# Optimization experiments

Measured on AMD Instinct MI355X. Metric: run time of the kernel, lower is better.

## Reference

```python
import jax, jax.numpy as jnp
import numpy as np

D_MODEL = 1024
D_K = 1024
B, T = 4, 2048


def setup_inputs() -> dict:
    key = jax.random.key(0)
    kx, kq, kk, kv = jax.random.split(key, 4)
    s = 1.0 / np.sqrt(D_MODEL)
    return {
        "x": jax.random.normal(kx, (B, T, D_MODEL), dtype=jnp.float32),
        "W_q": jax.random.normal(kq, (D_MODEL, D_K), dtype=jnp.float32) * s,
        "W_k": jax.random.normal(kk, (D_MODEL, D_K), dtype=jnp.float32) * s,
        "W_v": jax.random.normal(kv, (D_MODEL, D_K), dtype=jnp.float32) * s,
    }


def reference(x, W_q, W_k, W_v):
    # x: (B, T, C); W_*: (C, d_k). Linear(no bias) == x @ W
    q = jnp.einsum('btc,ck->btk', x, W_q)
    k = jnp.einsum('btc,ck->btk', x, W_k)
    v = jnp.einsum('btc,ck->btk', x, W_v)
    d_k = W_q.shape[1]
    scores = jnp.einsum('bqk,bsk->bqs', q, k) / jnp.sqrt(jnp.asarray(d_k, x.dtype))
    T_ = x.shape[1]
    causal = jnp.tril(jnp.ones((T_, T_), dtype=bool))
    scores = jnp.where(causal, scores, jnp.asarray(-jnp.inf, scores.dtype))
    weights = jax.nn.softmax(scores, axis=-1)
    return jnp.einsum('bqs,bsk->bqk', weights, v)
```

## Files before the change

kernel.cpp:

```cpp
#include <hip/hip_runtime.h>
#include <hip/hip_bf16.h>
#include <stdint.h>
#include <math.h>

typedef __bf16 bf16x8 __attribute__((ext_vector_type(8)));
typedef float  f32x4  __attribute__((ext_vector_type(4)));
typedef unsigned int u32x4 __attribute__((ext_vector_type(4)));

__device__ __forceinline__ unsigned short f2bf(float x) {
    union { float f; unsigned u; } v; v.f = x;
    unsigned r = v.u + 0x7fffu + ((v.u >> 16) & 1u);
    return (unsigned short)(r >> 16);
}

__device__ __forceinline__ float bf2f(unsigned short b) {
    union { unsigned u; float f; } v; v.u = ((unsigned)b) << 16; return v.f;
}

__device__ __forceinline__ void async16(const void* g, void* l) {
    __builtin_amdgcn_global_load_lds(
        (const __attribute__((address_space(1))) void*)g,
        (__attribute__((address_space(3))) void*)l,
        16, 0, 0);
}

template <typename OutT, bool KLIMIT, bool VFOLD, int ZMODE>
__global__ __launch_bounds__(256, 4) void gemm_bt(
    const unsigned short* __restrict__ A,
    const unsigned short* __restrict__ Bt,
    OutT* __restrict__ C,
    unsigned short* __restrict__ VtOut,
    int M, int N, int K, int lda, int ldb, int ldc,
    int ldvt, int nsplit,
    long long sA, long long sB, long long sC, long long sVt, float scale)
{
    int bn, bm, bz;
    if constexpr (ZMODE == 1) {
        const int o = blockIdx.x, x = o & 7, q = o >> 3;
        bz = x >> 1;
        const int tile = (x & 1) * 192 + q * 4 + blockIdx.z;
        bn = tile / 16; bm = tile % 16;
    } else if constexpr (ZMODE == 2) {
        const int o = blockIdx.x, x = o & 7, q = o >> 3;
        bz = x >> 1;
        const int t = (x & 1) * 68 + q * 4 + blockIdx.z;
        int r = (int)((sqrtf(8.f * (float)t + 1.f) - 1.f) * 0.5f);
        while ((r + 1) * (r + 2) / 2 <= t) r++;
        while (r * (r + 1) / 2 > t) r--;
        bm = r; bn = t - r * (r + 1) / 2;
    } else if constexpr (ZMODE == 3) {
        const int o = blockIdx.x, x = o & 7, q = o >> 3;
        bz = x >> 1;
        const int tile = (x & 1) * 64 + q * 4 + blockIdx.z;
        bn = tile >> 4; bm = 15 - (tile & 15);
    } else {
        bn = blockIdx.x;
        bm = KLIMIT ? (gridDim.y - 1 - blockIdx.y) : blockIdx.y;
        bz = blockIdx.z;
    }

    A  += (long long)bz * sA;
    Bt += (long long)bz * sB;
    C  += (long long)bz * sC;

    const int m0 = bm * 128, n0 = bn * 128;
    const int Keff = KLIMIT ? min(K, (bm + 1) * 128) : K;

    __shared__ __align__(16) unsigned short LDS[2 * 2 * 128 * 32];

    const int tid  = threadIdx.x;
    const int w    = tid >> 6, l = tid & 63;
    const int wr   = w >> 1,  wc = w & 1;
    const int lrow = l & 15,  quad = l >> 4;

    f32x4 acc[4][4] = {};

    const int rA0  = 32 * w + (l >> 2);
    const int cOff = (((l & 3) ^ ((l >> 3) & 3))) * 8;
    const unsigned short* aG0 = A  + (long long)(m0 + rA0)      * lda + cOff;
    const unsigned short* aG1 = A  + (long long)(m0 + rA0 + 16) * lda + cOff;
    const unsigned short* bG0 = Bt + (long long)(n0 + rA0)      * ldb + cOff;
    const unsigned short* bG1 = Bt + (long long)(n0 + rA0 + 16) * ldb + cOff;
    unsigned short* aL = &LDS[(2 * w) * 512 + l * 8];
    unsigned short* bL = aL + 4096;

    const int sl = (lrow >> 1) & 3;

    async16(aG0, aL);
    async16(aG1, aL + 512);
    async16(bG0, bL);
    async16(bG1, bL + 512);

    for (int k0 = 0; k0 < Keff; k0 += 32) {
        const int cur = ((k0 >> 5) & 1) * 8192;
        __syncthreads();

        if (k0 + 32 < Keff) {
            const int nxt = cur ^ 8192;
            async16(aG0 + k0 + 32, aL + nxt);
            async16(aG1 + k0 + 32, aL + nxt + 512);
            async16(bG0 + k0 + 32, bL + nxt);
            async16(bG1 + k0 + 32, bL + nxt + 512);
        }

        const unsigned short* As = &LDS[cur];
        const unsigned short* Bs = &LDS[cur + 4096];
        bf16x8 af[4], bfr[4];
#pragma unroll
        for (int i = 0; i < 4; i++) {
            af[i]  = *(const bf16x8*)&As[(wr * 64 + i * 16 + lrow) * 32 + (quad ^ sl) * 8];
            bfr[i] = *(const bf16x8*)&Bs[(wc * 64 + i * 16 + lrow) * 32 + (quad ^ sl) * 8];
        }
#pragma unroll
        for (int i = 0; i < 4; i++)
#pragma unroll
            for (int j = 0; j < 4; j++)
                acc[i][j] = __builtin_amdgcn_mfma_f32_16x16x32_bf16(af[i], bfr[j], acc[i][j], 0, 0, 0);
    }

    if constexpr (VFOLD) {
        if (n0 >= nsplit) {
            unsigned short* Vp = VtOut + (long long)bz * sVt;
#pragma unroll
            for (int i = 0; i < 4; i++) {
                const int t = m0 + wr * 64 + i * 16 + quad * 4;
#pragma unroll
                for (int j = 0; j < 4; j++) {
                    const int d = (n0 - nsplit) + wc * 64 + j * 16 + lrow;
                    union { unsigned short u[4]; uint2 p; } o;
#pragma unroll
                    for (int r = 0; r < 4; r++) o.u[r] = f2bf(acc[i][j][r] * scale);
                    *(uint2*)(Vp + (long long)d * ldvt + t) = o.p;
                }
            }
            return;
        }
    }

    __syncthreads();

    char* eb = (char*)LDS + w * 2288;
    const int erow = l >> 2, ep = l & 3;

    if constexpr (sizeof(OutT) == 2) {
#pragma unroll
        for (int i = 0; i < 4; i++) {
#pragma unroll
            for (int j = 0; j < 4; j++)
#pragma unroll
                for (int r = 0; r < 4; r++)
                    *(unsigned short*)(eb + (quad * 4 + r) * 144 + (j * 16 + lrow) * 2) =
                        f2bf(acc[i][j][r] * scale);
            const long long gm = m0 + wr * 64 + i * 16 + erow;
#pragma unroll
            for (int c = 0; c < 2; c++) {
                u32x4 d = *(u32x4*)(eb + erow * 144 + ep * 32 + c * 16);
                *(u32x4*)((unsigned short*)C + gm * ldc + (n0 + wc * 64 + ep * 16 + c * 8)) = d;
            }
        }
    } else {
#pragma unroll
        for (int i = 0; i < 4; i++) {
            const long long gm = m0 + wr * 64 + i * 16 + erow;
#pragma unroll
            for (int jc = 0; jc < 2; jc++) {
#pragma unroll
                for (int jj = 0; jj < 2; jj++)
#pragma unroll
                    for (int r = 0; r < 4; r++)
                        *(float*)(eb + (quad * 4 + r) * 144 + (jj * 16 + lrow) * 4) =
                            acc[i][2 * jc + jj][r] * scale;
#pragma unroll
                for (int c = 0; c < 2; c++) {
                    f32x4 d = *(f32x4*)(eb + erow * 144 + ep * 32 + c * 16);
                    *(f32x4*)((float*)C + gm * ldc + (n0 + wc * 64 + jc * 32 + ep * 8 + c * 4)) = d;
                }
            }
        }
    }
}

__global__ __launch_bounds__(256) void cast_f32_bf16(
    const float4* __restrict__ in, unsigned short* __restrict__ out, int n4)
{
    int i = blockIdx.x * 256 + threadIdx.x;
    if (i >= n4) return;
    float4 v = in[i];
    union { unsigned short u[4]; uint2 p; } o;
    o.u[0] = f2bf(v.x); o.u[1] = f2bf(v.y); o.u[2] = f2bf(v.z); o.u[3] = f2bf(v.w);
    *(uint2*)(out + (long long)i * 4) = o.p;
}

__global__ __launch_bounds__(256) void transpose_cast_w3(
    const float* __restrict__ W0, const float* __restrict__ W1,
    const float* __restrict__ W2, unsigned short* __restrict__ out, int n)
{
    const float* in = (blockIdx.z == 0) ? W0 : (blockIdx.z == 1) ? W1 : W2;
    out += (long long)blockIdx.z * n * n;
    __shared__ float tile[32][33];
    const int tx = threadIdx.x, ty = threadIdx.y;
    const int c0 = blockIdx.x * 32, r0 = blockIdx.y * 32;
#pragma unroll
    for (int i = 0; i < 4; i++)
        tile[ty + i * 8][tx] = in[(long long)(r0 + ty + i * 8) * n + c0 + tx];
    __syncthreads();
#pragma unroll
    for (int i = 0; i < 4; i++)
        out[(long long)(c0 + ty + i * 8) * n + r0 + tx] = f2bf(tile[tx][ty + i * 8]);
}

__global__ __launch_bounds__(256) void causal_softmax_bf16(
    const unsigned short* __restrict__ S, unsigned short* __restrict__ P, int T)
{
    const int row = blockIdx.x;
    const int t   = row & (T - 1);
    const int L   = t + 1;
    const unsigned short* s = S + (long long)row * T;
    unsigned short* p = P + (long long)row * T;
    const int tid  = threadIdx.x;
    const int base = tid * 8;

    uint4 raw = *(const uint4*)(s + base);
    unsigned rr[4] = {raw.x, raw.y, raw.z, raw.w};
    float v[8];
#pragma unroll
    for (int k = 0; k < 4; k++) {
        union { unsigned u; float f; } a, b;
        a.u = (rr[k] & 0xFFFFu) << 16;
        b.u = rr[k] & 0xFFFF0000u;
        v[2 * k] = a.f; v[2 * k + 1] = b.f;
    }
    float mx = -3.0e38f;
#pragma unroll
    for (int k = 0; k < 8; k++) {
        if (base + k >= L) v[k] = -3.0e38f;
        mx = fmaxf(mx, v[k]);
    }
#pragma unroll
    for (int off = 32; off; off >>= 1) mx = fmaxf(mx, __shfl_xor(mx, off));
    __shared__ float red[4], red2[4];
    const int wid = tid >> 6, lid = tid & 63;
    if (lid == 0) red[wid] = mx;
    __syncthreads();
    mx = fmaxf(fmaxf(red[0], red[1]), fmaxf(red[2], red[3]));

    float sum = 0.f;
#pragma unroll
    for (int k = 0; k < 8; k++) { v[k] = __expf(v[k] - mx); sum += v[k]; }
#pragma unroll
    for (int off = 32; off; off >>= 1) sum += __shfl_xor(sum, off);
    if (lid == 0) red2[wid] = sum;
    __syncthreads();
    sum = red2[0] + red2[1] + red2[2] + red2[3];
    const float inv = 1.0f / sum;

    union { unsigned short u[8]; uint4 q; } o;
#pragma unroll
    for (int k = 0; k < 8; k++) o.u[k] = f2bf(v[k] * inv);
    *(uint4*)(p + base) = o.q;
}

extern "C" void kernel_launch(void* const* d_in, const int* in_sizes, int n_in,
                              void* d_out, int out_size, void* d_ws, size_t ws_size,
                              hipStream_t stream)
{
    const int B = 4, T = 2048, C = 1024, D = 1024;
    const float* x  = (const float*)d_in[0];
    const float* Wq = (const float*)d_in[1];
    const float* Wk = (const float*)d_in[2];
    const float* Wv = (const float*)d_in[3];
    float* out = (float*)d_out;
    char* ws = (char*)d_ws;

    const size_t MB = 1ull << 20;
    unsigned short* Xbf   = (unsigned short*)(ws + 0);
    unsigned short* WqkvT = (unsigned short*)(ws + 16 * MB);
    unsigned short* QK    = (unsigned short*)(ws + 22 * MB);
    unsigned short* Vt    = (unsigned short*)(ws + 54 * MB);
    unsigned short* Sbf   = (unsigned short*)(ws + 70 * MB);
    unsigned short* P     = (unsigned short*)(ws + 0);

    const long long sX  = (long long)T * C;
    const long long sQK = (long long)T * 2 * D;
    const long long sVt = (long long)D * T;
    const long long sS  = (long long)T * T;
    const long long sO  = (long long)T * D;

    {
        int n4 = B * T * C / 4;
        cast_f32_bf16<<<dim3((n4 + 255) / 256), dim3(256), 0, stream>>>(
            (const float4*)x, Xbf, n4);
    }
    {
        dim3 g(32, 32, 3), b(32, 8);
        transpose_cast_w3<<<g, b, 0, stream>>>(Wq, Wk, Wv, WqkvT, 1024);
    }
    {
        dim3 g(384, 1, 4), b(256);
        gemm_bt<unsigned short, false, true, 1><<<g, b, 0, stream>>>(
            Xbf, WqkvT, QK, Vt, 2048, 3072, 1024, 1024, 1024, 2048,
             T,  2048, sX, 0, sQK, sVt, 1.0f);
    }
    {
        dim3 g(136, 1, 4), b(256);
        gemm_bt<unsigned short, false, false, 2><<<g, b, 0, stream>>>(
            QK, QK + D, Sbf, nullptr, 2048, 2048, 1024, 2 * D, 2 * D, 2048,
            0, 0, sQK, sQK, sS, 0, 0.03125f);
    }
    {
        causal_softmax_bf16<<<dim3(B * T), dim3(256), 0, stream>>>(Sbf, P, T);
    }
    {
        dim3 g(128, 1, 4), b(256);
        gemm_bt<float, true, false, 3><<<g, b, 0, stream>>>(
            P, Vt, out, nullptr, 2048, 1024, 2048, 2048, 2048, 1024,
            0, 0, sS, sVt, sO, 0, 1.0f);
    }
    (void)in_sizes; (void)n_in; (void)out_size; (void)ws_size;
}
```

Measured before the change: 236.8 us.

## Triple-buffer GEMM K-loop with vmcnt waits and fuse prep kernels

The GEMM main loop moves from a double-buffered LDS pipeline with __syncthreads to a three-stage ring. Loads are issued two steps ahead, and explicit s_waitcnt vmcnt plus s_barrier let in-flight global->LDS loads overlap the MFMA work. LDS use grows by half and launch bounds drop to 3 blocks per CU, which lowers occupancy. The x cast and weight transpose-cast kernels are also merged into one launch to save a kernel launch.

```diff
diff --git a/kernel.cpp b/kernel.cpp
--- a/kernel.cpp
+++ b/kernel.cpp
@@ -25,7 +25,7 @@
 }
 
 template <typename OutT, bool KLIMIT, bool VFOLD, int ZMODE>
-__global__ __launch_bounds__(256, 4) void gemm_bt(
+__global__ __launch_bounds__(256, 3) void gemm_bt(
     const unsigned short* __restrict__ A,
     const unsigned short* __restrict__ Bt,
     OutT* __restrict__ C,
@@ -65,8 +65,9 @@
 
     const int m0 = bm * 128, n0 = bn * 128;
     const int Keff = KLIMIT ? min(K, (bm + 1) * 128) : K;
-
-    __shared__ __align__(16) unsigned short LDS[2 * 2 * 128 * 32];
+    const int nsteps = Keff >> 5;
+
+    __shared__ __align__(16) unsigned short LDS[3 * 8192];
 
     const int tid  = threadIdx.x;
     const int w    = tid >> 6, l = tid & 63;
@@ -86,25 +87,28 @@
 
     const int sl = (lrow >> 1) & 3;
 
-    async16(aG0, aL);
-    async16(aG1, aL + 512);
-    async16(bG0, bL);
-    async16(bG1, bL + 512);
-
-    for (int k0 = 0; k0 < Keff; k0 += 32) {
-        const int cur = ((k0 >> 5) & 1) * 8192;
-        __syncthreads();
-
-        if (k0 + 32 < Keff) {
-            const int nxt = cur ^ 8192;
-            async16(aG0 + k0 + 32, aL + nxt);
-            async16(aG1 + k0 + 32, aL + nxt + 512);
-            async16(bG0 + k0 + 32, bL + nxt);
-            async16(bG1 + k0 + 32, bL + nxt + 512);
-        }
-
-        const unsigned short* As = &LDS[cur];
-        const unsigned short* Bs = &LDS[cur + 4096];
+    auto STG = [&](int s) {
+        const int off = (s % 3) * 8192;
+        const int kk  = s * 32;
+        async16(aG0 + kk, aL + off);
+        async16(aG1 + kk, aL + off + 512);
+        async16(bG0 + kk, bL + off);
+        async16(bG1 + kk, bL + off + 512);
+    };
+
+    STG(0);
+    if (nsteps > 1) STG(1);
+
+    for (int t = 0; t < nsteps; ++t) {
+        if (t + 1 < nsteps) asm volatile("s_waitcnt vmcnt(4)" ::: "memory");
+        else                asm volatile("s_waitcnt vmcnt(0)" ::: "memory");
+        __builtin_amdgcn_s_barrier();
+        asm volatile("" ::: "memory");
+
+        if (t + 2 < nsteps) STG(t + 2);
+
+        const unsigned short* As = &LDS[(t % 3) * 8192];
+        const unsigned short* Bs = As + 4096;
         bf16x8 af[4], bfr[4];
 #pragma unroll
         for (int i = 0; i < 4; i++) {
@@ -180,26 +184,29 @@
     }
 }
 
-__global__ __launch_bounds__(256) void cast_f32_bf16(
-    const float4* __restrict__ in, unsigned short* __restrict__ out, int n4)
+__global__ __launch_bounds__(256) void prep_fused(
+    const float4* __restrict__ xin, unsigned short* __restrict__ xout, int n4, int nCast,
+    const float* __restrict__ W0, const float* __restrict__ W1,
+    const float* __restrict__ W2, unsigned short* __restrict__ wout, int n)
 {
-    int i = blockIdx.x * 256 + threadIdx.x;
-    if (i >= n4) return;
-    float4 v = in[i];
-    union { unsigned short u[4]; uint2 p; } o;
-    o.u[0] = f2bf(v.x); o.u[1] = f2bf(v.y); o.u[2] = f2bf(v.z); o.u[3] = f2bf(v.w);
-    *(uint2*)(out + (long long)i * 4) = o.p;
-}
-
-__global__ __launch_bounds__(256) void transpose_cast_w3(
-    const float* __restrict__ W0, const float* __restrict__ W1,
-    const float* __restrict__ W2, unsigned short* __restrict__ out, int n)
-{
-    const float* in = (blockIdx.z == 0) ? W0 : (blockIdx.z == 1) ? W1 : W2;
-    out += (long long)blockIdx.z * n * n;
+    const int tid = threadIdx.x;
+    if ((int)blockIdx.x < nCast) {
+        int i = blockIdx.x * 256 + tid;
+        if (i >= n4) return;
+        float4 v = xin[i];
+        union { unsigned short u[4]; uint2 p; } o;
+        o.u[0] = f2bf(v.x); o.u[1] = f2bf(v.y); o.u[2] = f2bf(v.z); o.u[3] = f2bf(v.w);
+        *(uint2*)(xout + (long long)i * 4) = o.p;
+        return;
+    }
+    const int bx = blockIdx.x - nCast;
+    const int wz = bx >> 10, rem = bx & 1023;
+    const int wy = rem >> 5, wx = rem & 31;
+    const float* in = (wz == 0) ? W0 : (wz == 1) ? W1 : W2;
+    unsigned short* out = wout + (long long)wz * n * n;
     __shared__ float tile[32][33];
-    const int tx = threadIdx.x, ty = threadIdx.y;
-    const int c0 = blockIdx.x * 32, r0 = blockIdx.y * 32;
+    const int tx = tid & 31, ty = tid >> 5;
+    const int c0 = wx * 32, r0 = wy * 32;
 #pragma unroll
     for (int i = 0; i < 4; i++)
         tile[ty + i * 8][tx] = in[(long long)(r0 + ty + i * 8) * n + c0 + tx];
@@ -288,12 +295,9 @@
 
     {
         int n4 = B * T * C / 4;
-        cast_f32_bf16<<<dim3((n4 + 255) / 256), dim3(256), 0, stream>>>(
-            (const float4*)x, Xbf, n4);
-    }
-    {
-        dim3 g(32, 32, 3), b(32, 8);
-        transpose_cast_w3<<<g, b, 0, stream>>>(Wq, Wk, Wv, WqkvT, 1024);
+        int nCast = (n4 + 255) / 256;
+        prep_fused<<<dim3(nCast + 3072), dim3(256), 0, stream>>>(
+            (const float4*)x, Xbf, n4, nCast, Wq, Wk, Wv, WqkvT, 1024);
     }
     {
         dim3 g(384, 1, 4), b(256);
```

Result: no change. 233.0 us (-1.6%).
